# Kernel tuning notes

Measured on AMD Instinct MI355X. Metric: run time of the kernel, lower is better.

Reference implementation:

```python
import jax, jax.numpy as jnp
import numpy as np

REGION = (4, 4, 4)
NHEAD = 4
HEAD_DIM = 64
SCALE = HEAD_DIM ** -0.5
NUM_MODALITIES = 4


def _grid2seq(x, region, nhead):
    # x: [B, C, H, W, D] -> [B, nhead, n_regions, region_cube, head_dim]
    B, C, H, W, D = x.shape
    rh, rw, rd = H // region[0], W // region[1], D // region[2]
    hd = C // nhead
    x = x.reshape(B, nhead, hd, rh, region[0], rw, region[1], rd, region[2])
    x = x.transpose(0, 1, 3, 5, 7, 4, 6, 8, 2)  # bmchpwqdr -> bmhwdpqrc
    return x.reshape(B, nhead, rh * rw * rd, region[0] * region[1] * region[2], hd), rh, rw, rd


def _seq2grid(x, rh, rw, rd, region):
    # x: [B, nhead, n_regions, region_cube, head_dim] -> [B, C, H, W, D]
    B, nhead, nreg, rc, hd = x.shape
    x = x.reshape(B, nhead, rh, rw, rd, region[0], region[1], region[2], hd)
    x = x.transpose(0, 1, 8, 2, 5, 3, 6, 4, 7)  # bmhwdpqrc -> bmchpwqdr
    return x.reshape(B, nhead * hd, rh * region[0], rw * region[1], rd * region[2])


def _gather_regions(kv_seq, rg):
    # kv_seq: [B, H, kvN, kc, hd], rg: [B, H, qN, topk] -> [B, H, qN, topk, kc, hd]
    return jax.vmap(jax.vmap(lambda k, g: k[g]))(kv_seq, rg)


def setup_inputs() -> dict:
    key = jax.random.key(0)
    ks = jax.random.split(key, 20)
    shp = (2, 256, 16, 16, 16)
    inp = {"mask": jnp.ones((2, 4), dtype=jnp.int32)}
    names = [f"{p}{i}" for p in ("q", "k", "v") for i in range(4)]
    for n, kk in zip(names, ks[:12]):
        inp[n] = jax.random.normal(kk, shp, dtype=jnp.float32)
    for i, kk in zip(range(4), ks[12:16]):
        inp[f"rg{i}"] = jax.random.randint(kk, (2, 4, 64, 4), 0, 64, dtype=jnp.int32)
    return inp


def reference(mask, q0, q1, q2, q3, k0, k1, k2, k3, v0, v1, v2, v3, rg0, rg1, rg2, rg3):
    qs = [q0, q1, q2, q3]
    ks = [k0, k1, k2, k3]
    vs = [v0, v1, v2, v3]
    rgs = [rg0, rg1, rg2, rg3]

    q_seq, rh, rw, rd = zip(*[(g[0], g[1], g[2], g[3]) for g in [_grid2seq(q, REGION, NHEAD) for q in qs]])
    rh, rw, rd = rh[0], rw[0], rd[0]

    key_parts, val_parts = [], []
    for k_, v_, rg_ in zip(ks, vs, rgs):
        kseq, _, _, _ = _grid2seq(k_, REGION, NHEAD)
        vseq, _, _, _ = _grid2seq(v_, REGION, NHEAD)
        B, H, kvN, kc, hd = kseq.shape
        qN = rg_.shape[2]
        kg = _gather_regions(kseq, rg_).reshape(B, H, qN, -1, hd)  # [B,H,qN,topk*kc,hd]
        vg = _gather_regions(vseq, rg_).reshape(B, H, qN, -1, hd)
        key_parts.append(kg)
        val_parts.append(vg)
    key_g = jnp.concatenate(key_parts, axis=-2)  # [B,H,qN, M*topk*kc, hd]
    value_g = jnp.concatenate(val_parts, axis=-2)

    N = key_g.shape[-2]
    rep = N // NUM_MODALITIES
    mask_full = jnp.repeat(mask[:, None, None, None, :], rep, axis=-1)  # [B,1,1,1,N]

    outs = []
    for q in q_seq:
        attn = jnp.einsum("bhnqc,bhnkc->bhnqk", q * SCALE, key_g)
        attn = jnp.where(mask_full == 0, -jnp.inf, attn)
        attn = jax.nn.softmax(attn, axis=-1)
        o = jnp.einsum("bhnqk,bhnkc->bhnqc", attn, value_g)
        outs.append(_seq2grid(o, rh, rw, rd, REGION))
    return jnp.stack(outs, axis=0)  # [M, B, C, H, W, D]
```

## Files before the change

### kernel.cpp

```cpp
#include <hip/hip_runtime.h>
#include <hip/hip_bf16.h>

typedef short v8s __attribute__((ext_vector_type(8)));
typedef short v4s __attribute__((ext_vector_type(4)));
typedef float v4f __attribute__((ext_vector_type(4)));

#define LDK 72
#define SCALE_LOG2E 0.18033688f

struct MMRAParams {
    const float* q[4];
    const float* k[4];
    const float* v[4];
    const int*   rg[4];
    const int*   mask;
    float*       out;
};

__device__ __forceinline__ unsigned pkbf(float a, float b) {
    unsigned r;
    asm("v_cvt_pk_bf16_f32 %0, %1, %2" : "=v"(r) : "v"(a), "v"(b));
    return r;
}

__device__ __forceinline__ float fexp2(float x) {
#if __has_builtin(__builtin_amdgcn_exp2f)
    return __builtin_amdgcn_exp2f(x);
#else
    return exp2f(x);
#endif
}

__device__ __forceinline__ v4f mfma16(v4s a, v4s b, v4f c) {
#if __has_builtin(__builtin_amdgcn_mfma_f32_16x16x16bf16_1k)
    return __builtin_amdgcn_mfma_f32_16x16x16bf16_1k(a, b, c, 0, 0, 0);
#elif __has_builtin(__builtin_amdgcn_mfma_f32_16x16x16_bf16)
    return __builtin_amdgcn_mfma_f32_16x16x16_bf16(a, b, c, 0, 0, 0);
#else
    asm("v_mfma_f32_16x16x16_bf16 %0, %1, %2, %0" : "+v"(c) : "v"(a), "v"(b));
    return c;
#endif
}

__global__ __launch_bounds__(256, 2)
void mmra_attn(MMRAParams P) {
    const int bid = blockIdx.x;
    const int h = bid & 3;
    const int b = (bid >> 2) & 1;
    const int n = bid >> 3;
    const int H0 = ((n >> 4) & 3) << 2;
    const int W0 = ((n >> 2) & 3) << 2;
    const int D0 = (n & 3) << 2;

    const int tid  = threadIdx.x;
    const int wave = tid >> 6;
    const int lane = tid & 63;
    const int l15  = lane & 15;
    const int quad = lane >> 4;

    __shared__ __align__(16) ushort SMEM[18432];

    const int bh_base = (b * 256 + h * 64) * 4096;
    const int rgbase  = ((b * 4 + h) * 64 + n) * 4;

    const bool actm[4] = { P.mask[b * 4 + 0] != 0, P.mask[b * 4 + 1] != 0,
                           P.mask[b * 4 + 2] != 0, P.mask[b * 4 + 3] != 0 };

    auto kptr = [&](int m) { return (m == 0) ? P.k[0] : (m == 1) ? P.k[1] : (m == 2) ? P.k[2] : P.k[3]; };
    auto vptr = [&](int m) { return (m == 0) ? P.v[0] : (m == 1) ? P.v[1] : (m == 2) ? P.v[2] : P.v[3]; };
    auto rptr = [&](int m) { return (m == 0) ? P.rg[0] : (m == 1) ? P.rg[1] : (m == 2) ? P.rg[2] : P.rg[3]; };

    unsigned long long clist = 0ull; int nc = 0;
    for (int m = 0; m < 4; ++m) {
        if (actm[m]) {
            #pragma unroll
            for (int s = 0; s < 4; ++s) { clist |= ((unsigned long long)(m * 4 + s)) << (4 * nc); ++nc; }
        }
    }

    float4 pkf[4], pvf[4];
    auto prefetch = [&](int cj) {
        const int mod = cj >> 2, j = cj & 3;
        const int g = rptr(mod)[rgbase + j] & 63;
        const int goff = (((g >> 4) & 3) << 10) + (((g >> 2) & 3) << 6) + ((g & 3) << 2);
        const float* ks = kptr(mod);
        const float* vs = vptr(mod);
        const int off0 = bh_base + lane * 4096 + goff;
        #pragma unroll
        for (int i = 0; i < 4; ++i) {
            const int pq = wave * 4 + i;
            const int off = off0 + (pq >> 2) * 256 + (pq & 3) * 16;
            pkf[i] = *(const float4*)(ks + off);
            pvf[i] = *(const float4*)(vs + off);
        }
    };

    auto stage = [&](int buf) {
        ushort* Kb = SMEM + buf * 9216;
        ushort* Vb = Kb + 4608;
        #pragma unroll
        for (int i = 0; i < 4; ++i) {
            const int pq = wave * 4 + i;
            unsigned k01 = pkbf(pkf[i].x, pkf[i].y);
            unsigned k23 = pkbf(pkf[i].z, pkf[i].w);
            ushort* kb = &Kb[(pq * 4) * LDK + lane];
            kb[0 * LDK] = (ushort)k01;
            kb[1 * LDK] = (ushort)(k01 >> 16);
            kb[2 * LDK] = (ushort)k23;
            kb[3 * LDK] = (ushort)(k23 >> 16);
            uint2 vv;
            vv.x = pkbf(pvf[i].x, pvf[i].y);
            vv.y = pkbf(pvf[i].z, pvf[i].w);
            *(uint2*)&Vb[lane * LDK + pq * 4] = vv;
        }
    };

    prefetch((int)(clist & 15));

    v8s qfrag[4][2];
    {
        ushort* qbuf = SMEM + wave * 4608;
        const float* qsrc = (wave == 0) ? P.q[0] : (wave == 1) ? P.q[1] : (wave == 2) ? P.q[2] : P.q[3];
        #pragma unroll
        for (int rb = 0; rb < 4; ++rb) {
            #pragma unroll
            for (int i = 0; i < 4; ++i) {
                int off = bh_base + lane * 4096 + (H0 + rb) * 256 + (W0 + i) * 16 + D0;
                float4 cv = *(const float4*)(qsrc + off);
                unsigned q01 = pkbf(cv.x * SCALE_LOG2E, cv.y * SCALE_LOG2E);
                unsigned q23 = pkbf(cv.z * SCALE_LOG2E, cv.w * SCALE_LOG2E);
                ushort* qb = &qbuf[(rb * 16 + i * 4) * LDK + lane];
                qb[0 * LDK] = (ushort)q01;
                qb[1 * LDK] = (ushort)(q01 >> 16);
                qb[2 * LDK] = (ushort)q23;
                qb[3 * LDK] = (ushort)(q23 >> 16);
            }
        }
        __asm__ volatile("s_waitcnt lgkmcnt(0)" ::: "memory");
        #pragma unroll
        for (int rb = 0; rb < 4; ++rb) {
            qfrag[rb][0] = *(const v8s*)&qbuf[(rb * 16 + l15) * LDK + quad * 8];
            qfrag[rb][1] = *(const v8s*)&qbuf[(rb * 16 + l15) * LDK + 32 + quad * 8];
        }
    }
    __syncthreads();
    stage(0);
    if (nc > 1) prefetch((int)((clist >> 4) & 15));
    __syncthreads();

    v4f  oacc[4][4];
    float lrow[4];
    #pragma unroll
    for (int mt = 0; mt < 4; ++mt) {
        lrow[mt] = 0.f;
        #pragma unroll
        for (int t = 0; t < 4; ++t) oacc[mt][t] = (v4f){0.f, 0.f, 0.f, 0.f};
    }

    int cur = 0;
    #pragma unroll 1
    for (int i = 0; i < nc; ++i) {
        if (i + 1 < nc) {
            stage(cur ^ 1);
            if (i + 2 < nc) prefetch((int)((clist >> (4 * (i + 2))) & 15));
        }
        const ushort* Kb = SMEM + cur * 9216;
        const ushort* Vb = Kb + 4608;

        float sv[4][4][4];
        #pragma unroll
        for (int nt = 0; nt < 4; ++nt) {
            v8s kf0 = *(const v8s*)&Kb[(nt * 16 + l15) * LDK + quad * 8];
            v8s kf1 = *(const v8s*)&Kb[(nt * 16 + l15) * LDK + 32 + quad * 8];
            __builtin_amdgcn_s_setprio(1);
            #pragma unroll
            for (int mt = 0; mt < 4; ++mt) {
                v4f acc = (v4f){0.f, 0.f, 0.f, 0.f};
                acc = __builtin_amdgcn_mfma_f32_16x16x32_bf16(kf0, qfrag[mt][0], acc, 0, 0, 0);
                acc = __builtin_amdgcn_mfma_f32_16x16x32_bf16(kf1, qfrag[mt][1], acc, 0, 0, 0);
                #pragma unroll
                for (int r = 0; r < 4; ++r) sv[mt][nt][r] = acc[r];
            }
            __builtin_amdgcn_s_setprio(0);
        }
        uint2 pa[4][4];
        #pragma unroll
        for (int mt = 0; mt < 4; ++mt) {
            float rsum = 0.f;
            #pragma unroll
            for (int nt = 0; nt < 4; ++nt) {
                float p0 = fexp2(sv[mt][nt][0]);
                float p1 = fexp2(sv[mt][nt][1]);
                float p2 = fexp2(sv[mt][nt][2]);
                float p3 = fexp2(sv[mt][nt][3]);
                rsum += (p0 + p1) + (p2 + p3);
                pa[mt][nt].x = pkbf(p0, p1);
                pa[mt][nt].y = pkbf(p2, p3);
            }
            lrow[mt] += rsum;
        }

        __builtin_amdgcn_s_setprio(1);
        #pragma unroll
        for (int t = 0; t < 4; ++t) {
            #pragma unroll
            for (int nt = 0; nt < 4; ++nt) {
                v4s vf = *(const v4s*)&Vb[(t * 16 + l15) * LDK + nt * 16 + quad * 4];
                #pragma unroll
                for (int mt = 0; mt < 4; ++mt)
                    oacc[mt][t] = mfma16(__builtin_bit_cast(v4s, pa[mt][nt]), vf, oacc[mt][t]);
            }
        }
        __builtin_amdgcn_s_setprio(0);

        __syncthreads();
        cur ^= 1;
    }

    const int obase = (wave * 2 + b) * 1048576 + h * 64 * 4096;
    #pragma unroll
    for (int mt = 0; mt < 4; ++mt) {
        float lq = lrow[mt];
        lq += __shfl_xor(lq, 16);
        lq += __shfl_xor(lq, 32);
        const float invq = 1.0f / lq;
        float inv_row[4];
        #pragma unroll
        for (int r = 0; r < 4; ++r)
            inv_row[r] = __shfl(invq, (quad << 4) | (quad * 4 + r));
        #pragma unroll
        for (int t = 0; t < 4; ++t) {
            float4 ov;
            ov.x = oacc[mt][t][0] * inv_row[0];
            ov.y = oacc[mt][t][1] * inv_row[1];
            ov.z = oacc[mt][t][2] * inv_row[2];
            ov.w = oacc[mt][t][3] * inv_row[3];
            int off = obase + (t * 16 + l15) * 4096 + (H0 + mt) * 256 + (W0 + quad) * 16 + D0;
            *(float4*)(P.out + off) = ov;
        }
    }
}

extern "C" void kernel_launch(void* const* d_in, const int* in_sizes, int n_in,
                              void* d_out, int out_size, void* d_ws, size_t ws_size,
                              hipStream_t stream) {
    (void)in_sizes; (void)n_in; (void)out_size; (void)d_ws; (void)ws_size;
    MMRAParams P;
    P.mask = (const int*)d_in[0];
    for (int i = 0; i < 4; ++i) {
        P.q[i]  = (const float*)d_in[1 + i];
        P.k[i]  = (const float*)d_in[5 + i];
        P.v[i]  = (const float*)d_in[9 + i];
        P.rg[i] = (const int*)d_in[13 + i];
    }
    P.out = (float*)d_out;
    hipLaunchKernelGGL(mmra_attn, dim3(512), dim3(256), 0, stream, P);
}
```

Measured before the change: 218.7 us.

## Split key chunks across two wave groups and reduce partial outputs via LDS

Doubles the block to 512 threads. Two groups of four waves each process half of the gathered key/value chunks with separate double-buffered LDS regions. Group 1 writes its partial output accumulators and row sums to shared memory, and group 0 adds them before normalizing and storing. This shortens the serial chunk loop per wave and raises wave count. It costs doubled LDS, an extra reduction pass, and tighter register limits from the new launch bounds, which could cause spills.

```diff
diff --git a/kernel.cpp b/kernel.cpp
--- a/kernel.cpp
+++ b/kernel.cpp
@@ -42,7 +42,7 @@
 #endif
 }
 
-__global__ __launch_bounds__(256, 2)
+__global__ __launch_bounds__(512, 4)
 void mmra_attn(MMRAParams P) {
     const int bid = blockIdx.x;
     const int h = bid & 3;
@@ -54,11 +54,13 @@
 
     const int tid  = threadIdx.x;
     const int wave = tid >> 6;
+    const int qm   = wave & 3;
+    const int ch   = wave >> 2;
     const int lane = tid & 63;
     const int l15  = lane & 15;
     const int quad = lane >> 4;
 
-    __shared__ __align__(16) ushort SMEM[18432];
+    __shared__ __align__(16) ushort SMEM[36864];
 
     const int bh_base = (b * 256 + h * 64) * 4096;
     const int rgbase  = ((b * 4 + h) * 64 + n) * 4;
@@ -77,6 +79,8 @@
             for (int s = 0; s < 4; ++s) { clist |= ((unsigned long long)(m * 4 + s)) << (4 * nc); ++nc; }
         }
     }
+    const int nch = nc >> 1;
+    auto chunkAt = [&](int i) { return (int)((clist >> (4 * i)) & 15); };
 
     float4 pkf[4], pvf[4];
     auto prefetch = [&](int cj) {
@@ -88,19 +92,19 @@
         const int off0 = bh_base + lane * 4096 + goff;
         #pragma unroll
         for (int i = 0; i < 4; ++i) {
-            const int pq = wave * 4 + i;
+            const int pq = qm * 4 + i;
             const int off = off0 + (pq >> 2) * 256 + (pq & 3) * 16;
             pkf[i] = *(const float4*)(ks + off);
             pvf[i] = *(const float4*)(vs + off);
         }
     };
 
-    auto stage = [&](int buf) {
-        ushort* Kb = SMEM + buf * 9216;
+    auto stage = [&](int sbuf) {
+        ushort* Kb = SMEM + sbuf * 9216;
         ushort* Vb = Kb + 4608;
         #pragma unroll
         for (int i = 0; i < 4; ++i) {
-            const int pq = wave * 4 + i;
+            const int pq = qm * 4 + i;
             unsigned k01 = pkbf(pkf[i].x, pkf[i].y);
             unsigned k23 = pkbf(pkf[i].z, pkf[i].w);
             ushort* kb = &Kb[(pq * 4) * LDK + lane];
@@ -115,12 +119,12 @@
         }
     };
 
-    prefetch((int)(clist & 15));
+    prefetch(chunkAt(ch * nch));
 
     v8s qfrag[4][2];
     {
         ushort* qbuf = SMEM + wave * 4608;
-        const float* qsrc = (wave == 0) ? P.q[0] : (wave == 1) ? P.q[1] : (wave == 2) ? P.q[2] : P.q[3];
+        const float* qsrc = (qm == 0) ? P.q[0] : (qm == 1) ? P.q[1] : (qm == 2) ? P.q[2] : P.q[3];
         #pragma unroll
         for (int rb = 0; rb < 4; ++rb) {
             #pragma unroll
@@ -144,8 +148,8 @@
         }
     }
     __syncthreads();
-    stage(0);
-    if (nc > 1) prefetch((int)((clist >> 4) & 15));
+    stage(ch * 2);
+    if (nch > 1) prefetch(chunkAt(ch * nch + 1));
     __syncthreads();
 
     v4f  oacc[4][4];
@@ -159,12 +163,12 @@
 
     int cur = 0;
     #pragma unroll 1
-    for (int i = 0; i < nc; ++i) {
-        if (i + 1 < nc) {
-            stage(cur ^ 1);
-            if (i + 2 < nc) prefetch((int)((clist >> (4 * (i + 2))) & 15));
-        }
-        const ushort* Kb = SMEM + cur * 9216;
+    for (int i = 0; i < nch; ++i) {
+        if (i + 1 < nch) {
+            stage(ch * 2 + (cur ^ 1));
+            if (i + 2 < nch) prefetch(chunkAt(ch * nch + i + 2));
+        }
+        const ushort* Kb = SMEM + (ch * 2 + cur) * 9216;
         const ushort* Vb = Kb + 4608;
 
         float sv[4][4][4];
@@ -217,26 +221,56 @@
         cur ^= 1;
     }
 
-    const int obase = (wave * 2 + b) * 1048576 + h * 64 * 4096;
+    float lqv[4];
     #pragma unroll
     for (int mt = 0; mt < 4; ++mt) {
         float lq = lrow[mt];
         lq += __shfl_xor(lq, 16);
         lq += __shfl_xor(lq, 32);
-        const float invq = 1.0f / lq;
-        float inv_row[4];
-        #pragma unroll
-        for (int r = 0; r < 4; ++r)
-            inv_row[r] = __shfl(invq, (quad << 4) | (quad * 4 + r));
-        #pragma unroll
-        for (int t = 0; t < 4; ++t) {
-            float4 ov;
-            ov.x = oacc[mt][t][0] * inv_row[0];
-            ov.y = oacc[mt][t][1] * inv_row[1];
-            ov.z = oacc[mt][t][2] * inv_row[2];
-            ov.w = oacc[mt][t][3] * inv_row[3];
-            int off = obase + (t * 16 + l15) * 4096 + (H0 + mt) * 256 + (W0 + quad) * 16 + D0;
-            *(float4*)(P.out + off) = ov;
+        lqv[mt] = lq;
+    }
+    float* FS = (float*)SMEM;
+    const int xb = (qm * 68) * 64 + lane;
+    if (ch == 1) {
+        #pragma unroll
+        for (int mt = 0; mt < 4; ++mt) {
+            #pragma unroll
+            for (int t = 0; t < 4; ++t)
+                #pragma unroll
+                for (int r = 0; r < 4; ++r)
+                    FS[xb + (mt * 16 + t * 4 + r) * 64] = oacc[mt][t][r];
+            FS[xb + (64 + mt) * 64] = lqv[mt];
+        }
+    }
+    __syncthreads();
+    if (ch == 0) {
+        #pragma unroll
+        for (int mt = 0; mt < 4; ++mt) {
+            #pragma unroll
+            for (int t = 0; t < 4; ++t)
+                #pragma unroll
+                for (int r = 0; r < 4; ++r)
+                    oacc[mt][t][r] += FS[xb + (mt * 16 + t * 4 + r) * 64];
+            lqv[mt] += FS[xb + (64 + mt) * 64];
+        }
+        const int obase = (qm * 2 + b) * 1048576 + h * 64 * 4096;
+        #pragma unroll
+        for (int mt = 0; mt < 4; ++mt) {
+            const float invq = 1.0f / lqv[mt];
+            float inv_row[4];
+            #pragma unroll
+            for (int r = 0; r < 4; ++r)
+                inv_row[r] = __shfl(invq, (quad << 4) | (quad * 4 + r));
+            #pragma unroll
+            for (int t = 0; t < 4; ++t) {
+                float4 ov;
+                ov.x = oacc[mt][t][0] * inv_row[0];
+                ov.y = oacc[mt][t][1] * inv_row[1];
+                ov.z = oacc[mt][t][2] * inv_row[2];
+                ov.w = oacc[mt][t][3] * inv_row[3];
+                int off = obase + (t * 16 + l15) * 4096 + (H0 + mt) * 256 + (W0 + quad) * 16 + D0;
+                *(float4*)(P.out + off) = ov;
+            }
         }
     }
 }
@@ -254,5 +288,5 @@
         P.rg[i] = (const int*)d_in[13 + i];
     }
     P.out = (float*)d_out;
-    hipLaunchKernelGGL(mmra_attn, dim3(512), dim3(256), 0, stream, P);
-}
+    hipLaunchKernelGGL(mmra_attn, dim3(512), dim3(512), 0, stream, P);
+}
```

Measured after the change: 516.3 us. 2.36x slower.
